# Optimization experiments

Measured on AMD Instinct MI355X. Metric: run time of the kernel, lower is better.

## Reference

```python
import jax, jax.numpy as jnp
import numpy as np
from jax import lax

TEMP = 0.05
MOMENTUM = 0.9
EPS = 1e-12


def _l2_normalize(x, axis=-1):
    n = jnp.sqrt(jnp.sum(x * x, axis=axis, keepdims=True))
    return x / jnp.maximum(n, EPS)


def _cross_entropy(logits, targets):
    # mean over batch of -log_softmax(logits)[target]
    logp = jax.nn.log_softmax(logits, axis=-1)
    return -jnp.mean(jnp.take_along_axis(logp, targets[:, None], axis=-1))


def _momentum_update(features, x, targets, m):
    # Sequential per-sample read-modify-write (faithful to the torch loop,
    # matters when targets contain duplicates). carry = memory bank.
    def step(f, xy):
        x_i, y_i = xy
        row = m * f[y_i] + (1.0 - m) * x_i
        row = row / jnp.linalg.norm(row)
        return f.at[y_i].set(row), None
    f, _ = lax.scan(step, features, (x, targets))
    return f


def setup_inputs() -> dict:
    key = jax.random.key(0)
    k1, k2, k3, k4, k5, k6 = jax.random.split(key, 6)
    B, D, N = 512, 1024, 16384
    inputs_rgb = jax.random.normal(k1, (B, D), dtype=jnp.float32)
    inputs_ir = jax.random.normal(k2, (B, D), dtype=jnp.float32)
    targets_rgb = jax.random.randint(k3, (B,), 0, N, dtype=jnp.int32)
    targets_ir = jax.random.randint(k4, (B,), 0, N, dtype=jnp.int32)
    # memory banks (buffers); initialized as normalized random rows to mimic a
    # warmed-up cluster memory (the module starts at zeros, degenerate for CE)
    features_rgb = _l2_normalize(jax.random.normal(k5, (N, D), dtype=jnp.float32))
    features_ir = _l2_normalize(jax.random.normal(k6, (N, D), dtype=jnp.float32))
    return {"inputs_rgb": inputs_rgb, "inputs_ir": inputs_ir,
            "targets_rgb": targets_rgb, "targets_ir": targets_ir,
            "features_rgb": features_rgb, "features_ir": features_ir}


def reference(inputs_rgb, inputs_ir, targets_rgb, targets_ir, features_rgb, features_ir):
    x_rgb = _l2_normalize(inputs_rgb)  # [B, D]
    x_ir = _l2_normalize(inputs_ir)
    logits_rgb = (x_rgb @ features_rgb.T) / TEMP  # [B, N]
    logits_ir = (x_ir @ features_ir.T) / TEMP
    loss_rgb = _cross_entropy(logits_rgb, targets_rgb)
    loss_ir = _cross_entropy(logits_ir, targets_ir)
    # side-effect of CM.backward in the original: momentum scatter update + renorm
    # (change_scale == 1.0 so the Hungarian cross-modal exchange is skipped)
    new_features_rgb = _momentum_update(features_rgb, x_rgb, targets_rgb, MOMENTUM)
    new_features_ir = _momentum_update(features_ir, x_ir, targets_ir, MOMENTUM)
    return (loss_rgb, loss_ir, new_features_rgb, new_features_ir)
```

## Files before the change

### kernel.cpp

```cpp
#include <hip/hip_runtime.h>
#include <math.h>

#define BATCH 512
#define DIM   1024
#define NCLUS 16384
#define TINV  20.0f

typedef __attribute__((ext_vector_type(4))) float f32x4;
typedef __attribute__((ext_vector_type(8))) short bf16x8;

static __device__ __forceinline__ unsigned short f2bf(float f) {
  unsigned int u = __float_as_uint(f);
  u += 0x7FFFu + ((u >> 16) & 1u);
  return (unsigned short)(u >> 16);
}

typedef const __attribute__((address_space(1))) unsigned int* gas1_t;
typedef __attribute__((address_space(3))) unsigned int* las3_t;
static __device__ __forceinline__ void gload16(const void* g, void* l) {
  __builtin_amdgcn_global_load_lds((gas1_t)g, (las3_t)l, 16, 0, 0);
}

__global__ void nrm_kernel(const float* __restrict__ in_rgb,
                           const float* __restrict__ in_ir,
                           float* __restrict__ xf,
                           unsigned short* __restrict__ xb,
                           float* __restrict__ accum) {
  int gid = blockIdx.x * blockDim.x + threadIdx.x;
  if (gid < 2048) accum[gid] = 0.0f;

  int row = blockIdx.x;
  int mod = row >> 9;
  int r   = row & 511;
  const float* in = (mod ? in_ir : in_rgb) + (size_t)r * DIM;
  float* xo          = xf + ((size_t)mod * BATCH + r) * DIM;
  unsigned short* xbo = xb + ((size_t)mod * BATCH + r) * DIM;

  int t = threadIdx.x;
  float4 v = ((const float4*)in)[t];
  float ss = v.x*v.x + v.y*v.y + v.z*v.z + v.w*v.w;
#pragma unroll
  for (int m = 1; m < 64; m <<= 1) ss += __shfl_xor(ss, m, 64);
  __shared__ float red[4];
  if ((t & 63) == 0) red[t >> 6] = ss;
  __syncthreads();
  float inv = 1.0f / fmaxf(sqrtf(red[0] + red[1] + red[2] + red[3]), 1e-12f);
  float4 o = make_float4(v.x * inv, v.y * inv, v.z * inv, v.w * inv);
  ((float4*)xo)[t] = o;
  ushort4 ob = make_ushort4(f2bf(o.x), f2bf(o.y), f2bf(o.z), f2bf(o.w));
  ((ushort4*)xbo)[t] = ob;
}

__global__ void cvtcopy_kernel(const float* __restrict__ f_rgb,
                               const float* __restrict__ f_ir,
                               float* __restrict__ out,
                               unsigned short* __restrict__ fb,
                               int precvt) {
  const size_t n4 = (size_t)NCLUS * DIM / 4;
  size_t stride = (size_t)gridDim.x * blockDim.x;
  for (size_t i = (size_t)blockIdx.x * blockDim.x + threadIdx.x; i < 2 * n4; i += stride) {
    const float4 v = (i < n4) ? ((const float4*)f_rgb)[i] : ((const float4*)f_ir)[i - n4];
    float2* o2 = (float2*)(out + 4 * i);
    o2[0] = make_float2(v.x, v.y);
    o2[1] = make_float2(v.z, v.w);
    if (precvt)
      ((ushort4*)fb)[i] = make_ushort4(f2bf(v.x), f2bf(v.y), f2bf(v.z), f2bf(v.w));
  }
}

#define BM 128
#define BN 128
#define BK 32

template<int PRECVT>
__global__ void gemm_lse_kernel(const unsigned short* __restrict__ xb,
                                const unsigned short* __restrict__ fb,
                                const float* __restrict__ f_rgb,
                                const float* __restrict__ f_ir,
                                const int* __restrict__ t_rgb,
                                const int* __restrict__ t_ir,
                                float* __restrict__ rowsum,
                                float* __restrict__ tgtlog) {
  const int nt  = blockIdx.x;
  const int bt  = blockIdx.y & 3;
  const int mod = blockIdx.y >> 2;

  const unsigned short* X  = xb + ((size_t)mod * BATCH + bt * BM) * DIM;
  const unsigned short* Bb = fb + ((size_t)mod * NCLUS + nt * BN) * DIM;
  const float* Ff = (mod ? f_ir : f_rgb) + (size_t)nt * BN * DIM;
  const int*   tg = mod ? t_ir : t_rgb;
  float* rs = rowsum + mod * BATCH;
  float* tl = tgtlog + mod * BATCH;

  __shared__ __align__(16) unsigned short As[BM * BK];
  __shared__ __align__(16) unsigned short Bs[BN * BK];

  const int tid  = threadIdx.x;
  const int wid  = tid >> 6;
  const int lane = tid & 63;
  const int wr = wid >> 1, wc = wid & 1;
  const int l15 = lane & 15, lhi = lane >> 4;

  f32x4 acc[4][4];
#pragma unroll
  for (int m = 0; m < 4; ++m)
#pragma unroll
    for (int n = 0; n < 4; ++n) acc[m][n] = (f32x4){0.f, 0.f, 0.f, 0.f};

  for (int kk = 0; kk < DIM; kk += BK) {
#pragma unroll
    for (int i = 0; i < 2; ++i) {
      int q = i * 256 + tid;
      gload16(X + (size_t)(q >> 2) * DIM + kk + (q & 3) * 8,
              As + (size_t)(i * 256 + wid * 64) * 8);
      if (PRECVT)
        gload16(Bb + (size_t)(q >> 2) * DIM + kk + (q & 3) * 8,
                Bs + (size_t)(i * 256 + wid * 64) * 8);
    }
    if (!PRECVT) {
#pragma unroll
      for (int i = 0; i < 4; ++i) {
        int id = i * 256 + tid;
        int row = id >> 3, c4 = (id & 7) << 2;
        float4 v = *(const float4*)(Ff + (size_t)row * DIM + kk + c4);
        *(ushort4*)(&Bs[row * BK + c4]) =
            make_ushort4(f2bf(v.x), f2bf(v.y), f2bf(v.z), f2bf(v.w));
      }
    }
    __syncthreads();

    bf16x8 a[4], b[4];
#pragma unroll
    for (int m = 0; m < 4; ++m)
      a[m] = *(const bf16x8*)(&As[(wr * 64 + m * 16 + l15) * BK + lhi * 8]);
#pragma unroll
    for (int n = 0; n < 4; ++n)
      b[n] = *(const bf16x8*)(&Bs[(wc * 64 + n * 16 + l15) * BK + lhi * 8]);
#pragma unroll
    for (int m = 0; m < 4; ++m)
#pragma unroll
      for (int n = 0; n < 4; ++n)
        acc[m][n] = __builtin_amdgcn_mfma_f32_16x16x32_bf16(a[m], b[n], acc[m][n], 0, 0, 0);
    __syncthreads();
  }

#pragma unroll
  for (int m = 0; m < 4; ++m) {
    const int browbase = bt * BM + wr * 64 + m * 16 + lhi * 4;
    float esum[4];
#pragma unroll
    for (int j = 0; j < 4; ++j) {
      const int brow = browbase + j;
      const int t = tg[brow];
      float e = 0.f;
#pragma unroll
      for (int n = 0; n < 4; ++n) {
        float logit = acc[m][n][j] * TINV;
        e += __expf(logit);
        int col = nt * BN + wc * 64 + n * 16 + l15;
        if (col == t) tl[brow] = logit;
      }
      esum[j] = e;
    }
#pragma unroll
    for (int j = 0; j < 4; ++j) {
      float e = esum[j];
      e += __shfl_xor(e, 1, 64);
      e += __shfl_xor(e, 2, 64);
      e += __shfl_xor(e, 4, 64);
      e += __shfl_xor(e, 8, 64);
      if (l15 == 0) atomicAdd(rs + browbase + j, e);
    }
  }
}

__global__ void loss_kernel(const float* __restrict__ rowsum,
                            const float* __restrict__ tgtlog,
                            float* __restrict__ out) {
  int t = threadIdx.x;
  float lr = logf(rowsum[t]) - tgtlog[t];
  float li = logf(rowsum[BATCH + t]) - tgtlog[BATCH + t];
#pragma unroll
  for (int m = 1; m < 64; m <<= 1) { lr += __shfl_xor(lr, m, 64); li += __shfl_xor(li, m, 64); }
  __shared__ float sr[8], si[8];
  if ((t & 63) == 0) { sr[t >> 6] = lr; si[t >> 6] = li; }
  __syncthreads();
  if (t == 0) {
    float a = 0.f, b = 0.f;
#pragma unroll
    for (int i = 0; i < 8; ++i) { a += sr[i]; b += si[i]; }
    out[0] = a * (1.0f / BATCH);
    out[1] = b * (1.0f / BATCH);
  }
}

__global__ void mom_kernel(const int* __restrict__ t_rgb,
                           const int* __restrict__ t_ir,
                           const float* __restrict__ xf,
                           float* __restrict__ out) {
  const int i   = blockIdx.x;
  const int mod = blockIdx.y;
  const int* tg = mod ? t_ir : t_rgb;
  const int y = tg[i];
  for (int j = 0; j < i; ++j)
    if (tg[j] == y) return;

  const float* x = xf + (size_t)mod * BATCH * DIM;
  float* rowp = out + (size_t)mod * NCLUS * DIM + (size_t)y * DIM;

  const int t = threadIdx.x;
  float2 r0 = ((const float2*)rowp)[t];
  float2 r1 = ((const float2*)rowp)[t + 256];
  __shared__ float red[4];

  for (int j = i; j < BATCH; ++j) {
    if (tg[j] != y) continue;
    const float2* xr = (const float2*)(x + (size_t)j * DIM);
    float2 x0 = xr[t], x1 = xr[t + 256];
    r0.x = 0.9f * r0.x + 0.1f * x0.x;
    r0.y = 0.9f * r0.y + 0.1f * x0.y;
    r1.x = 0.9f * r1.x + 0.1f * x1.x;
    r1.y = 0.9f * r1.y + 0.1f * x1.y;
    float ss = r0.x*r0.x + r0.y*r0.y + r1.x*r1.x + r1.y*r1.y;
#pragma unroll
    for (int m = 1; m < 64; m <<= 1) ss += __shfl_xor(ss, m, 64);
    if ((t & 63) == 0) red[t >> 6] = ss;
    __syncthreads();
    float tot = red[0] + red[1] + red[2] + red[3];
    __syncthreads();
    float inv = 1.0f / sqrtf(tot);
    r0.x *= inv; r0.y *= inv; r1.x *= inv; r1.y *= inv;
  }
  ((float2*)rowp)[t] = r0;
  ((float2*)rowp)[t + 256] = r1;
}

extern "C" void kernel_launch(void* const* d_in, const int* in_sizes, int n_in,
                              void* d_out, int out_size, void* d_ws, size_t ws_size,
                              hipStream_t stream) {
  (void)in_sizes; (void)n_in; (void)out_size;
  const float* in_rgb = (const float*)d_in[0];
  const float* in_ir  = (const float*)d_in[1];
  const int*   t_rgb  = (const int*)d_in[2];
  const int*   t_ir   = (const int*)d_in[3];
  const float* f_rgb  = (const float*)d_in[4];
  const float* f_ir   = (const float*)d_in[5];
  float* out = (float*)d_out;

  char* ws = (char*)d_ws;
  float*          xf     = (float*)ws;
  unsigned short* xb     = (unsigned short*)(ws + (4u<<20));
  float*          rowsum = (float*)(ws + (6u<<20));
  float*          tgtlog = rowsum + 1024;
  unsigned short* fb     = (unsigned short*)(ws + (8u<<20));
  const int precvt = (ws_size >= ((size_t)72 << 20)) ? 1 : 0;

  nrm_kernel<<<1024, 256, 0, stream>>>(in_rgb, in_ir, xf, xb, rowsum);
  cvtcopy_kernel<<<2048, 256, 0, stream>>>(f_rgb, f_ir, out + 2, fb, precvt);
  if (precvt)
    gemm_lse_kernel<1><<<dim3(128, 8), 256, 0, stream>>>(xb, fb, f_rgb, f_ir,
                                                         t_rgb, t_ir, rowsum, tgtlog);
  else
    gemm_lse_kernel<0><<<dim3(128, 8), 256, 0, stream>>>(xb, fb, f_rgb, f_ir,
                                                         t_rgb, t_ir, rowsum, tgtlog);
  mom_kernel<<<dim3(512, 2), 256, 0, stream>>>(t_rgb, t_ir, xf, out + 2);
  loss_kernel<<<1, 512, 0, stream>>>(rowsum, tgtlog, out);
}
```

Measured before the change: 189.5 us.

## Rewrite GEMM-LSE as 256x256 tile with 4-stage LDS pipeline and swizzle

```diff
diff --git a/kernel.cpp b/kernel.cpp
--- a/kernel.cpp
+++ b/kernel.cpp
@@ -7,6 +7,7 @@
 #define TINV  20.0f
 
 typedef __attribute__((ext_vector_type(4))) float f32x4;
+typedef __attribute__((ext_vector_type(2))) float f32x2;
 typedef __attribute__((ext_vector_type(8))) short bf16x8;
 
 static __device__ __forceinline__ unsigned short f2bf(float f) {
@@ -54,99 +55,128 @@
 __global__ void cvtcopy_kernel(const float* __restrict__ f_rgb,
                                const float* __restrict__ f_ir,
                                float* __restrict__ out,
-                               unsigned short* __restrict__ fb,
-                               int precvt) {
+                               unsigned short* __restrict__ fb) {
   const size_t n4 = (size_t)NCLUS * DIM / 4;
   size_t stride = (size_t)gridDim.x * blockDim.x;
   for (size_t i = (size_t)blockIdx.x * blockDim.x + threadIdx.x; i < 2 * n4; i += stride) {
-    const float4 v = (i < n4) ? ((const float4*)f_rgb)[i] : ((const float4*)f_ir)[i - n4];
-    float2* o2 = (float2*)(out + 4 * i);
-    o2[0] = make_float2(v.x, v.y);
-    o2[1] = make_float2(v.z, v.w);
-    if (precvt)
-      ((ushort4*)fb)[i] = make_ushort4(f2bf(v.x), f2bf(v.y), f2bf(v.z), f2bf(v.w));
-  }
-}
-
-#define BM 128
-#define BN 128
+    const f32x4* src = (i < n4) ? ((const f32x4*)f_rgb) + i
+                                : ((const f32x4*)f_ir) + (i - n4);
+    const f32x4 v = __builtin_nontemporal_load(src);
+    f32x2* o2 = (f32x2*)(out + 4 * i);
+    __builtin_nontemporal_store((f32x2){v.x, v.y}, o2);
+    __builtin_nontemporal_store((f32x2){v.z, v.w}, o2 + 1);
+    ((ushort4*)fb)[i] = make_ushort4(f2bf(v.x), f2bf(v.y), f2bf(v.z), f2bf(v.w));
+  }
+}
+
+#define BM 256
+#define BN 256
 #define BK 32
-
-template<int PRECVT>
+#define KT_N (DIM / BK)
+
+__launch_bounds__(512, 2)
 __global__ void gemm_lse_kernel(const unsigned short* __restrict__ xb,
                                 const unsigned short* __restrict__ fb,
-                                const float* __restrict__ f_rgb,
-                                const float* __restrict__ f_ir,
                                 const int* __restrict__ t_rgb,
                                 const int* __restrict__ t_ir,
                                 float* __restrict__ rowsum,
                                 float* __restrict__ tgtlog) {
   const int nt  = blockIdx.x;
-  const int bt  = blockIdx.y & 3;
-  const int mod = blockIdx.y >> 2;
-
-  const unsigned short* X  = xb + ((size_t)mod * BATCH + bt * BM) * DIM;
-  const unsigned short* Bb = fb + ((size_t)mod * NCLUS + nt * BN) * DIM;
-  const float* Ff = (mod ? f_ir : f_rgb) + (size_t)nt * BN * DIM;
-  const int*   tg = mod ? t_ir : t_rgb;
+  const int bt  = blockIdx.y & 1;
+  const int mod = blockIdx.y >> 1;
+
+  const unsigned short* X = xb + ((size_t)mod * BATCH + bt * BM) * DIM;
+  const unsigned short* F = fb + ((size_t)mod * NCLUS + (size_t)nt * BN) * DIM;
+  const int* tg = mod ? t_ir : t_rgb;
   float* rs = rowsum + mod * BATCH;
   float* tl = tgtlog + mod * BATCH;
 
-  __shared__ __align__(16) unsigned short As[BM * BK];
-  __shared__ __align__(16) unsigned short Bs[BN * BK];
+  __shared__ __align__(16) unsigned short Ab[4][BM * BK];
+  __shared__ __align__(16) unsigned short Bb[4][BN * BK];
 
   const int tid  = threadIdx.x;
   const int wid  = tid >> 6;
   const int lane = tid & 63;
-  const int wr = wid >> 1, wc = wid & 1;
+  const int wr = wid >> 2, wc = wid & 3;
   const int l15 = lane & 15, lhi = lane >> 4;
-
-  f32x4 acc[4][4];
-#pragma unroll
-  for (int m = 0; m < 4; ++m)
+  const int sw = (l15 & 6) << 3;
+
+  f32x4 acc[8][4];
+#pragma unroll
+  for (int m = 0; m < 8; ++m)
 #pragma unroll
     for (int n = 0; n < 4; ++n) acc[m][n] = (f32x4){0.f, 0.f, 0.f, 0.f};
 
-  for (int kk = 0; kk < DIM; kk += BK) {
-#pragma unroll
-    for (int i = 0; i < 2; ++i) {
-      int q = i * 256 + tid;
-      gload16(X + (size_t)(q >> 2) * DIM + kk + (q & 3) * 8,
-              As + (size_t)(i * 256 + wid * 64) * 8);
-      if (PRECVT)
-        gload16(Bb + (size_t)(q >> 2) * DIM + kk + (q & 3) * 8,
-                Bs + (size_t)(i * 256 + wid * 64) * 8);
-    }
-    if (!PRECVT) {
-#pragma unroll
-      for (int i = 0; i < 4; ++i) {
-        int id = i * 256 + tid;
-        int row = id >> 3, c4 = (id & 7) << 2;
-        float4 v = *(const float4*)(Ff + (size_t)row * DIM + kk + c4);
-        *(ushort4*)(&Bs[row * BK + c4]) =
-            make_ushort4(f2bf(v.x), f2bf(v.y), f2bf(v.z), f2bf(v.w));
-      }
-    }
-    __syncthreads();
-
+  auto STAGE_A = [&](int sl, int kt) {
+#pragma unroll
+    for (int c = 0; c < 2; ++c) {
+      int q = c * 512 + tid;
+      int cs = (q & 3) ^ ((q >> 3) & 3);
+      gload16(X + (size_t)(q >> 2) * DIM + kt * BK + cs * 8,
+              &Ab[sl][(c * 512 + wid * 64) * 8]);
+    }
+  };
+  auto STAGE_B = [&](int sl, int kt) {
+#pragma unroll
+    for (int c = 0; c < 2; ++c) {
+      int q = c * 512 + tid;
+      int cs = (q & 3) ^ ((q >> 3) & 3);
+      gload16(F + (size_t)(q >> 2) * DIM + kt * BK + cs * 8,
+              &Bb[sl][(c * 512 + wid * 64) * 8]);
+    }
+  };
+  auto LDA = [&](int sl, int row) {
+    return *(const bf16x8*)((const char*)Ab[sl] + ((row * (BK * 2) + lhi * 16) ^ sw));
+  };
+  auto LDB = [&](int sl, int row) {
+    return *(const bf16x8*)((const char*)Bb[sl] + ((row * (BK * 2) + lhi * 16) ^ sw));
+  };
+
+  auto ITERATION = [&](int i, bool doStage, bool vm4) {
+    const int sl = i & 3, sp = (i + 2) & 3;
     bf16x8 a[4], b[4];
 #pragma unroll
-    for (int m = 0; m < 4; ++m)
-      a[m] = *(const bf16x8*)(&As[(wr * 64 + m * 16 + l15) * BK + lhi * 8]);
-#pragma unroll
-    for (int n = 0; n < 4; ++n)
-      b[n] = *(const bf16x8*)(&Bs[(wc * 64 + n * 16 + l15) * BK + lhi * 8]);
+    for (int n = 0; n < 4; ++n) b[n] = LDB(sl, wc * 64 + n * 16 + l15);
+#pragma unroll
+    for (int m = 0; m < 4; ++m) a[m] = LDA(sl, wr * 128 + m * 16 + l15);
+    if (doStage) STAGE_A(sp, i + 2);
+    __builtin_amdgcn_s_barrier();
+    __builtin_amdgcn_s_setprio(1);
 #pragma unroll
     for (int m = 0; m < 4; ++m)
 #pragma unroll
       for (int n = 0; n < 4; ++n)
         acc[m][n] = __builtin_amdgcn_mfma_f32_16x16x32_bf16(a[m], b[n], acc[m][n], 0, 0, 0);
-    __syncthreads();
-  }
-
-#pragma unroll
-  for (int m = 0; m < 4; ++m) {
-    const int browbase = bt * BM + wr * 64 + m * 16 + lhi * 4;
+    __builtin_amdgcn_s_setprio(0);
+    __builtin_amdgcn_s_barrier();
+#pragma unroll
+    for (int m = 0; m < 4; ++m) a[m] = LDA(sl, wr * 128 + 64 + m * 16 + l15);
+    if (doStage) STAGE_B(sp, i + 2);
+    __builtin_amdgcn_s_barrier();
+    __builtin_amdgcn_s_setprio(1);
+#pragma unroll
+    for (int m = 0; m < 4; ++m)
+#pragma unroll
+      for (int n = 0; n < 4; ++n)
+        acc[m + 4][n] = __builtin_amdgcn_mfma_f32_16x16x32_bf16(a[m], b[n], acc[m + 4][n], 0, 0, 0);
+    __builtin_amdgcn_s_setprio(0);
+    if (vm4) asm volatile("s_waitcnt vmcnt(4)" ::: "memory");
+    else     asm volatile("s_waitcnt vmcnt(0)" ::: "memory");
+    __builtin_amdgcn_s_barrier();
+  };
+
+  STAGE_A(0, 0); STAGE_B(0, 0);
+  STAGE_A(1, 1); STAGE_B(1, 1);
+  asm volatile("s_waitcnt vmcnt(4)" ::: "memory");
+  __builtin_amdgcn_s_barrier();
+
+  for (int i = 0; i < KT_N - 2; ++i) ITERATION(i, true, true);
+  ITERATION(KT_N - 2, false, false);
+  ITERATION(KT_N - 1, false, false);
+
+#pragma unroll
+  for (int M = 0; M < 8; ++M) {
+    const int browbase = bt * BM + wr * 128 + ((M >> 2) << 6) + ((M & 3) << 4) + (lhi << 2);
     float esum[4];
 #pragma unroll
     for (int j = 0; j < 4; ++j) {
@@ -155,7 +185,7 @@
       float e = 0.f;
 #pragma unroll
       for (int n = 0; n < 4; ++n) {
-        float logit = acc[m][n][j] * TINV;
+        float logit = acc[M][n][j] * TINV;
         e += __expf(logit);
         int col = nt * BN + wc * 64 + n * 16 + l15;
         if (col == t) tl[brow] = logit;
@@ -238,7 +268,7 @@
 extern "C" void kernel_launch(void* const* d_in, const int* in_sizes, int n_in,
                               void* d_out, int out_size, void* d_ws, size_t ws_size,
                               hipStream_t stream) {
-  (void)in_sizes; (void)n_in; (void)out_size;
+  (void)in_sizes; (void)n_in; (void)out_size; (void)ws_size;
   const float* in_rgb = (const float*)d_in[0];
   const float* in_ir  = (const float*)d_in[1];
   const int*   t_rgb  = (const int*)d_in[2];
@@ -253,16 +283,10 @@
   float*          rowsum = (float*)(ws + (6u<<20));
   float*          tgtlog = rowsum + 1024;
   unsigned short* fb     = (unsigned short*)(ws + (8u<<20));
-  const int precvt = (ws_size >= ((size_t)72 << 20)) ? 1 : 0;
 
   nrm_kernel<<<1024, 256, 0, stream>>>(in_rgb, in_ir, xf, xb, rowsum);
-  cvtcopy_kernel<<<2048, 256, 0, stream>>>(f_rgb, f_ir, out + 2, fb, precvt);
-  if (precvt)
-    gemm_lse_kernel<1><<<dim3(128, 8), 256, 0, stream>>>(xb, fb, f_rgb, f_ir,
-                                                         t_rgb, t_ir, rowsum, tgtlog);
-  else
-    gemm_lse_kernel<0><<<dim3(128, 8), 256, 0, stream>>>(xb, fb, f_rgb, f_ir,
-                                                         t_rgb, t_ir, rowsum, tgtlog);
+  cvtcopy_kernel<<<2048, 256, 0, stream>>>(f_rgb, f_ir, out + 2, fb);
+  gemm_lse_kernel<<<dim3(64, 4), 512, 0, stream>>>(xb, fb, t_rgb, t_ir, rowsum, tgtlog);
   mom_kernel<<<dim3(512, 2), 256, 0, stream>>>(t_rgb, t_ir, xf, out + 2);
   loss_kernel<<<1, 512, 0, stream>>>(rowsum, tgtlog, out);
 }
```

Result: slower. 193.9 us (+2.3%).
